# Kernel tuning notes

Measured on AMD Instinct MI355X. Metric: run time of the kernel, lower is better.

The kernel has to match this reference:

```python
import jax, jax.numpy as jnp
import numpy as np

N_NODES = 100000
N_EDGES = 3200000
D_IN = 128
D_OUT = 128


def setup_inputs() -> dict:
    key = jax.random.key(0)
    k1, k2, k3, k4, k5, k6 = jax.random.split(key, 6)
    x = jax.random.normal(k1, (N_NODES, D_IN), dtype=jnp.float32)
    edge_row = jnp.sort(jax.random.randint(k2, (N_EDGES,), 0, N_NODES, dtype=jnp.int32))
    edge_col = jax.random.randint(k3, (N_EDGES,), 0, N_NODES, dtype=jnp.int32)
    edge_val = jax.random.uniform(k4, (N_EDGES,), dtype=jnp.float32)
    stdv = 1.0 / np.sqrt(D_OUT)
    weight = jax.random.uniform(k5, (D_IN, D_OUT), dtype=jnp.float32, minval=-stdv, maxval=stdv)
    bias = jax.random.uniform(k6, (D_OUT,), dtype=jnp.float32, minval=-stdv, maxval=stdv)
    return {"x": x, "edge_row": edge_row, "edge_col": edge_col,
            "edge_val": edge_val, "weight": weight, "bias": bias}


def reference(x, edge_row, edge_col, edge_val, weight, bias):
    # support = A @ x  (sparse COO SpMM via gather + segment-sum scatter)
    gathered = x[edge_col] * edge_val[:, None]          # [E, D_IN]
    support = jax.ops.segment_sum(gathered, edge_row, num_segments=N_NODES)  # [N, D_IN]
    # output = support @ W + b
    return support @ weight + bias
```

## Files before the change

kernel.cpp:

```cpp
#include <hip/hip_runtime.h>

#define NNODES 100000
#define NEDGES 3200000
#define DIM    128

typedef __bf16  bf16x8 __attribute__((ext_vector_type(8)));
typedef unsigned short u16;
typedef u16     u16x8  __attribute__((ext_vector_type(8)));
typedef float   f32x4  __attribute__((ext_vector_type(4)));
typedef unsigned int u32;
typedef u32     u32x4  __attribute__((ext_vector_type(4)));

__device__ __forceinline__ u16 f2bf(float f) {
    union { float f; unsigned int i; } c;
    c.f = f;
    unsigned int x = c.i;
    unsigned int rounding = 0x7fff + ((x >> 16) & 1);
    x += rounding;
    return (u16)(x >> 16);
}

__device__ __forceinline__ float asf(u32 u) {
    union { u32 i; float f; } c; c.i = u; return c.f;
}

__device__ __forceinline__ bf16x8 ldfrag_u16(const u16* p) {
    u16x8 u = *(const u16x8*)p;
    return __builtin_bit_cast(bf16x8, u);
}

__device__ __forceinline__ bf16x8 ldfrag_f32(const float* p) {
    f32x4 a = *(const f32x4*)p;
    f32x4 b = *(const f32x4*)(p + 4);
    u16x8 u;
#pragma unroll
    for (int i = 0; i < 4; ++i) u[i] = f2bf(a[i]);
#pragma unroll
    for (int i = 0; i < 4; ++i) u[4 + i] = f2bf(b[i]);
    return __builtin_bit_cast(bf16x8, u);
}

__global__ void build_row_ptr(const int* __restrict__ edge_row,
                              int* __restrict__ row_ptr) {
    int n = blockIdx.x * blockDim.x + threadIdx.x;
    if (n > NNODES) return;
    int lo = 0, hi = NEDGES;
    while (lo < hi) {
        int mid = (lo + hi) >> 1;
        if (edge_row[mid] < n) lo = mid + 1; else hi = mid;
    }
    row_ptr[n] = lo;
}

__global__ void prep_wt(const float* __restrict__ w, u16* __restrict__ wt) {
    int i = blockIdx.x * blockDim.x + threadIdx.x;
    if (i >= DIM * DIM) return;
    int k = i >> 7, n = i & 127;
    wt[n * DIM + k] = f2bf(w[k * DIM + n]);
}

#define WT_STRIDE 136
__global__ __launch_bounds__(256) void gemm_xw(const float* __restrict__ x,
                                               const u16* __restrict__ wt,
                                               u16* __restrict__ y) {
    __shared__ u16 wlds[DIM * WT_STRIDE];
    __shared__ u16 ybounce[4][16 * DIM];

    int tid = threadIdx.x;
    {
        const f32x4* src = (const f32x4*)wt;
#pragma unroll
        for (int i = 0; i < 8; ++i) {
            int ci  = tid + 256 * i;
            int row = ci >> 4, off = ci & 15;
            *((f32x4*)(wlds + row * WT_STRIDE) + off) = src[ci];
        }
    }
    __syncthreads();

    int wave = __builtin_amdgcn_readfirstlane(tid >> 6);
    int lane = tid & 63;
    int quad = lane >> 4, l16 = lane & 15;
    int mBase = (blockIdx.x * 4 + wave) * 16;
    if (mBase >= NNODES) return;

    const float* xrow = x + (size_t)(mBase + l16) * DIM + quad * 8;

    f32x4 acc[8];
#pragma unroll
    for (int nt = 0; nt < 8; ++nt) acc[nt] = (f32x4){0.f, 0.f, 0.f, 0.f};

#pragma unroll
    for (int kb = 0; kb < 4; ++kb) {
        bf16x8 a = ldfrag_f32(xrow + kb * 32);
#pragma unroll
        for (int nt = 0; nt < 8; ++nt) {
            bf16x8 b = ldfrag_u16(wlds + (nt * 16 + l16) * WT_STRIDE + kb * 32 + quad * 8);
            acc[nt] = __builtin_amdgcn_mfma_f32_16x16x32_bf16(a, b, acc[nt], 0, 0, 0);
        }
    }

    u16* yb = ybounce[wave];
#pragma unroll
    for (int nt = 0; nt < 8; ++nt) {
        int col = nt * 16 + l16;
#pragma unroll
        for (int r = 0; r < 4; ++r)
            yb[(quad * 4 + r) * DIM + col] = f2bf(acc[nt][r]);
    }
#pragma unroll
    for (int j = 0; j < 4; ++j) {
        int lr = j * 4 + quad;
        u16x8 t = *(const u16x8*)(yb + lr * DIM + l16 * 8);
        *(u16x8*)(y + (size_t)(mBase + lr) * DIM + l16 * 8) = t;
    }
}

__global__ __launch_bounds__(256, 8) void spmm(const int* __restrict__ row_ptr,
                                               const int* __restrict__ ecol,
                                               const float* __restrict__ eval,
                                               const u16* __restrict__ y,
                                               const float* __restrict__ bias,
                                               float* __restrict__ out) {
    int lane = threadIdx.x & 63;
    int row  = __builtin_amdgcn_readfirstlane(blockIdx.x * 4 + (threadIdx.x >> 6));
    if (row >= NNODES) return;

    int lo = row_ptr[row];
    int hi = row_ptr[row + 1];

    int grp = lane >> 4;
    int sub = lane & 15;

    float acc[8];
#pragma unroll
    for (int j = 0; j < 8; ++j) acc[j] = 0.f;

    const u16* ychunk = y + sub * 8;

    int e = lo;
    for (; e + 16 <= hi; e += 16) {
#pragma unroll
        for (int b = 0; b < 4; ++b) {
            int e0 = e + b * 4;
            int   c0 = ecol[e0], c1 = ecol[e0 + 1], c2 = ecol[e0 + 2], c3 = ecol[e0 + 3];
            float v0 = eval[e0], v1 = eval[e0 + 1], v2 = eval[e0 + 2], v3 = eval[e0 + 3];
            int   c = grp < 2 ? (grp == 0 ? c0 : c1) : (grp == 2 ? c2 : c3);
            float v = grp < 2 ? (grp == 0 ? v0 : v1) : (grp == 2 ? v2 : v3);
            u32x4 q = *(const u32x4*)(ychunk + (size_t)c * DIM);
#pragma unroll
            for (int j = 0; j < 4; ++j) {
                acc[2 * j]     += v * asf(q[j] << 16);
                acc[2 * j + 1] += v * asf(q[j] & 0xffff0000u);
            }
        }
    }
    for (; e < hi; e += 4) {
        int rem = hi - e;
        int i1 = rem > 1 ? e + 1 : e, i2 = rem > 2 ? e + 2 : e, i3 = rem > 3 ? e + 3 : e;
        int   c0 = ecol[e],  c1 = ecol[i1], c2 = ecol[i2], c3 = ecol[i3];
        float v0 = eval[e];
        float v1 = rem > 1 ? eval[i1] : 0.f;
        float v2 = rem > 2 ? eval[i2] : 0.f;
        float v3 = rem > 3 ? eval[i3] : 0.f;
        int   c = grp < 2 ? (grp == 0 ? c0 : c1) : (grp == 2 ? c2 : c3);
        float v = grp < 2 ? (grp == 0 ? v0 : v1) : (grp == 2 ? v2 : v3);
        u32x4 q = *(const u32x4*)(ychunk + (size_t)c * DIM);
#pragma unroll
        for (int j = 0; j < 4; ++j) {
            acc[2 * j]     += v * asf(q[j] << 16);
            acc[2 * j + 1] += v * asf(q[j] & 0xffff0000u);
        }
    }

#pragma unroll
    for (int j = 0; j < 8; ++j) {
        acc[j] += __shfl_xor(acc[j], 16);
        acc[j] += __shfl_xor(acc[j], 32);
    }

    if (grp == 0) {
        float* orow = out + (size_t)row * DIM + sub * 8;
        f32x4 o0, o1;
#pragma unroll
        for (int j = 0; j < 4; ++j) {
            o0[j] = acc[j]     + bias[sub * 8 + j];
            o1[j] = acc[4 + j] + bias[sub * 8 + 4 + j];
        }
        __builtin_nontemporal_store(o0, (f32x4*)orow);
        __builtin_nontemporal_store(o1, (f32x4*)(orow + 4));
    }
}

extern "C" void kernel_launch(void* const* d_in, const int* in_sizes, int n_in,
                              void* d_out, int out_size, void* d_ws, size_t ws_size,
                              hipStream_t stream) {
    const float* x        = (const float*)d_in[0];
    const int*   edge_row = (const int*)d_in[1];
    const int*   edge_col = (const int*)d_in[2];
    const float* edge_val = (const float*)d_in[3];
    const float* weight   = (const float*)d_in[4];
    const float* bias     = (const float*)d_in[5];
    float* out = (float*)d_out;

    char* ws = (char*)d_ws;
    u16* y       = (u16*)ws;
    int* row_ptr = (int*)(ws + (size_t)NNODES * DIM * 2);
    u16* wt      = (u16*)(ws + 26000128);

    prep_wt<<<(DIM * DIM + 255) / 256, 256, 0, stream>>>(weight, wt);
    build_row_ptr<<<(NNODES + 1 + 255) / 256, 256, 0, stream>>>(edge_row, row_ptr);

    gemm_xw<<<(NNODES / 16 + 3) / 4, 256, 0, stream>>>(x, wt, y);

    spmm<<<NNODES / 4, 256, 0, stream>>>(row_ptr, edge_col, edge_val, y, bias, out);
}
```

Before: 246.6 us.

## Merge prep kernels, reuse LDS for output bounce, hoist x loads, split spmm launch

Merges the weight transpose and row_ptr binary search into one prep kernel to save a launch. The gemm now loads all x fragments up front, uses hardware bf16 conversion, reuses the weight LDS buffer as the output bounce buffer so occupancy can rise (launch bounds 256,4), and writes y with nontemporal stores. The spmm is split into two half-range launches with a row offset, which adds a launch without an obvious benefit. The extra __syncthreads and the active-flag predication replace the early return in the gemm.

```diff
diff --git a/kernel.cpp b/kernel.cpp
--- a/kernel.cpp
+++ b/kernel.cpp
@@ -11,13 +11,9 @@
 typedef unsigned int u32;
 typedef u32     u32x4  __attribute__((ext_vector_type(4)));
 
-__device__ __forceinline__ u16 f2bf(float f) {
-    union { float f; unsigned int i; } c;
-    c.f = f;
-    unsigned int x = c.i;
-    unsigned int rounding = 0x7fff + ((x >> 16) & 1);
-    x += rounding;
-    return (u16)(x >> 16);
+__device__ __forceinline__ u16 bfbits(float f) {
+    __bf16 h = (__bf16)f;
+    return __builtin_bit_cast(u16, h);
 }
 
 __device__ __forceinline__ float asf(u32 u) {
@@ -29,42 +25,38 @@
     return __builtin_bit_cast(bf16x8, u);
 }
 
-__device__ __forceinline__ bf16x8 ldfrag_f32(const float* p) {
-    f32x4 a = *(const f32x4*)p;
-    f32x4 b = *(const f32x4*)(p + 4);
-    u16x8 u;
-#pragma unroll
-    for (int i = 0; i < 4; ++i) u[i] = f2bf(a[i]);
-#pragma unroll
-    for (int i = 0; i < 4; ++i) u[4 + i] = f2bf(b[i]);
-    return __builtin_bit_cast(bf16x8, u);
-}
-
-__global__ void build_row_ptr(const int* __restrict__ edge_row,
-                              int* __restrict__ row_ptr) {
-    int n = blockIdx.x * blockDim.x + threadIdx.x;
-    if (n > NNODES) return;
-    int lo = 0, hi = NEDGES;
-    while (lo < hi) {
-        int mid = (lo + hi) >> 1;
-        if (edge_row[mid] < n) lo = mid + 1; else hi = mid;
-    }
-    row_ptr[n] = lo;
-}
-
-__global__ void prep_wt(const float* __restrict__ w, u16* __restrict__ wt) {
-    int i = blockIdx.x * blockDim.x + threadIdx.x;
-    if (i >= DIM * DIM) return;
-    int k = i >> 7, n = i & 127;
-    wt[n * DIM + k] = f2bf(w[k * DIM + n]);
+__device__ __forceinline__ bf16x8 cvt8(f32x4 a, f32x4 b) {
+    bf16x8 r;
+#pragma unroll
+    for (int i = 0; i < 4; ++i) {
+        r[i]     = (__bf16)a[i];
+        r[4 + i] = (__bf16)b[i];
+    }
+    return r;
+}
+
+__global__ void prep(const int* __restrict__ edge_row, int* __restrict__ row_ptr,
+                     const float* __restrict__ w, u16* __restrict__ wt) {
+    int gid = blockIdx.x * blockDim.x + threadIdx.x;
+    if (gid <= NNODES) {
+        int lo = 0, hi = NEDGES;
+        while (lo < hi) {
+            int mid = (lo + hi) >> 1;
+            if (edge_row[mid] < gid) lo = mid + 1; else hi = mid;
+        }
+        row_ptr[gid] = lo;
+    }
+    if (gid < DIM * DIM) {
+        int k = gid >> 7, n = gid & 127;
+        wt[n * DIM + k] = bfbits(w[k * DIM + n]);
+    }
 }
 
 #define WT_STRIDE 136
-__global__ __launch_bounds__(256) void gemm_xw(const float* __restrict__ x,
-                                               const u16* __restrict__ wt,
-                                               u16* __restrict__ y) {
+__global__ __launch_bounds__(256, 4) void gemm_xw(const float* __restrict__ x,
+                                                  const u16* __restrict__ wt,
+                                                  u16* __restrict__ y) {
     __shared__ u16 wlds[DIM * WT_STRIDE];
-    __shared__ u16 ybounce[4][16 * DIM];
 
     int tid = threadIdx.x;
     {
@@ -82,37 +74,52 @@
     int lane = tid & 63;
     int quad = lane >> 4, l16 = lane & 15;
     int mBase = (blockIdx.x * 4 + wave) * 16;
-    if (mBase >= NNODES) return;
+    int active = (mBase < NNODES);
 
     const float* xrow = x + (size_t)(mBase + l16) * DIM + quad * 8;
 
+    f32x4 xa[4], xb[4];
+    if (active) {
+#pragma unroll
+        for (int kb = 0; kb < 4; ++kb) {
+            xa[kb] = *(const f32x4*)(xrow + kb * 32);
+            xb[kb] = *(const f32x4*)(xrow + kb * 32 + 4);
+        }
+    }
+
     f32x4 acc[8];
 #pragma unroll
     for (int nt = 0; nt < 8; ++nt) acc[nt] = (f32x4){0.f, 0.f, 0.f, 0.f};
 
-#pragma unroll
-    for (int kb = 0; kb < 4; ++kb) {
-        bf16x8 a = ldfrag_f32(xrow + kb * 32);
+    if (active) {
+#pragma unroll
+        for (int kb = 0; kb < 4; ++kb) {
+            bf16x8 a = cvt8(xa[kb], xb[kb]);
+#pragma unroll
+            for (int nt = 0; nt < 8; ++nt) {
+                bf16x8 b = ldfrag_u16(wlds + (nt * 16 + l16) * WT_STRIDE + kb * 32 + quad * 8);
+                acc[nt] = __builtin_amdgcn_mfma_f32_16x16x32_bf16(a, b, acc[nt], 0, 0, 0);
+            }
+        }
+    }
+
+    __syncthreads();
+
+    if (active) {
+        u16* yb = wlds + wave * (16 * DIM);
 #pragma unroll
         for (int nt = 0; nt < 8; ++nt) {
-            bf16x8 b = ldfrag_u16(wlds + (nt * 16 + l16) * WT_STRIDE + kb * 32 + quad * 8);
-            acc[nt] = __builtin_amdgcn_mfma_f32_16x16x32_bf16(a, b, acc[nt], 0, 0, 0);
-        }
-    }
-
-    u16* yb = ybounce[wave];
-#pragma unroll
-    for (int nt = 0; nt < 8; ++nt) {
-        int col = nt * 16 + l16;
-#pragma unroll
-        for (int r = 0; r < 4; ++r)
-            yb[(quad * 4 + r) * DIM + col] = f2bf(acc[nt][r]);
-    }
-#pragma unroll
-    for (int j = 0; j < 4; ++j) {
-        int lr = j * 4 + quad;
-        u16x8 t = *(const u16x8*)(yb + lr * DIM + l16 * 8);
-        *(u16x8*)(y + (size_t)(mBase + lr) * DIM + l16 * 8) = t;
+            int col = nt * 16 + l16;
+#pragma unroll
+            for (int r = 0; r < 4; ++r)
+                yb[(quad * 4 + r) * DIM + col] = bfbits(acc[nt][r]);
+        }
+#pragma unroll
+        for (int j = 0; j < 4; ++j) {
+            int lr = j * 4 + quad;
+            u16x8 t = *(const u16x8*)(yb + lr * DIM + l16 * 8);
+            __builtin_nontemporal_store(t, (u16x8*)(y + (size_t)(mBase + lr) * DIM + l16 * 8));
+        }
     }
 }
 
@@ -121,9 +128,10 @@
                                                const float* __restrict__ eval,
                                                const u16* __restrict__ y,
                                                const float* __restrict__ bias,
-                                               float* __restrict__ out) {
+                                               float* __restrict__ out,
+                                               int rowBase) {
     int lane = threadIdx.x & 63;
-    int row  = __builtin_amdgcn_readfirstlane(blockIdx.x * 4 + (threadIdx.x >> 6));
+    int row  = __builtin_amdgcn_readfirstlane(rowBase + blockIdx.x * 4 + (threadIdx.x >> 6));
     if (row >= NNODES) return;
 
     int lo = row_ptr[row];
@@ -208,10 +216,10 @@
     int* row_ptr = (int*)(ws + (size_t)NNODES * DIM * 2);
     u16* wt      = (u16*)(ws + 26000128);
 
-    prep_wt<<<(DIM * DIM + 255) / 256, 256, 0, stream>>>(weight, wt);
-    build_row_ptr<<<(NNODES + 1 + 255) / 256, 256, 0, stream>>>(edge_row, row_ptr);
+    prep<<<(NNODES + 1 + 255) / 256, 256, 0, stream>>>(edge_row, row_ptr, weight, wt);
 
     gemm_xw<<<(NNODES / 16 + 3) / 4, 256, 0, stream>>>(x, wt, y);
 
-    spmm<<<NNODES / 4, 256, 0, stream>>>(row_ptr, edge_col, edge_val, y, bias, out);
-}
+    spmm<<<NNODES / 8, 256, 0, stream>>>(row_ptr, edge_col, edge_val, y, bias, out, 0);
+    spmm<<<NNODES / 8, 256, 0, stream>>>(row_ptr, edge_col, edge_val, y, bias, out, NNODES / 2);
+}
```

Measured after the change: 252.7 us. 1.02x slower.
